# Optimization experiments

Hardware: AMD Instinct MI355X
Metric: run time of the kernel (lower is better)

Reference implementation:

```python
import jax, jax.numpy as jnp
import numpy as np

B, T, D_IN, D_PROJ = 256, 2048, 25, 128


def setup_inputs() -> dict:
    key = jax.random.key(0)
    ks = jax.random.split(key, 7)
    s1 = 1.0 / np.sqrt(D_IN)
    s2 = 1.0 / np.sqrt(D_PROJ)
    return {
        "x": jax.random.normal(ks[0], (B, T, D_IN), dtype=jnp.float32),
        "ln_gamma": jnp.ones((D_IN,), dtype=jnp.float32),
        "ln_beta": jnp.zeros((D_IN,), dtype=jnp.float32),
        "w1": jax.random.uniform(ks[1], (D_IN, D_PROJ), jnp.float32, -s1, s1),
        "b1": jax.random.uniform(ks[2], (D_PROJ,), jnp.float32, -s1, s1),
        "w2": jax.random.uniform(ks[3], (D_PROJ, D_PROJ), jnp.float32, -s2, s2),
        "b2": jax.random.uniform(ks[4], (D_PROJ,), jnp.float32, -s2, s2),
    }


def reference(x, ln_gamma, ln_beta, w1, b1, w2, b2):
    # LayerNorm over last dim (eps=1e-5, torch default)
    mu = jnp.mean(x, axis=-1, keepdims=True)
    var = jnp.mean(jnp.square(x - mu), axis=-1, keepdims=True)
    xn = (x - mu) * jax.lax.rsqrt(var + 1e-5) * ln_gamma + ln_beta
    h = jnp.einsum("btd,dp->btp", xn, w1) + b1
    h = jax.nn.gelu(h, approximate=False)  # torch nn.GELU default = exact erf
    return jnp.einsum("btp,pq->btq", h, w2) + b2
```

## Files before the change

### kernel.cpp

```cpp
#include <hip/hip_runtime.h>
#include <hip/hip_bf16.h>
#include <stdint.h>

#define BT    (256*2048)
#define DIN   25
#define DP    128
#define MTILE 128
#define NBLK  (BT/MTILE)
#define HSTR  136

typedef __attribute__((ext_vector_type(8))) __bf16          bf16x8;
typedef __attribute__((ext_vector_type(8))) unsigned short  u16x8;
typedef __attribute__((ext_vector_type(4))) float           f32x4;

#define SM_H     0
#define SM_XN    34816
#define SM_SMALL (34816 + 8192)
#define SM_BYTES (SM_SMALL + 306*4)

__device__ __forceinline__ unsigned short f2bf(float f) {
  unsigned int u = __float_as_uint(f);
  u += 0x7fffu + ((u >> 16) & 1u);
  return (unsigned short)(u >> 16);
}

__device__ __forceinline__ float gelu_exact(float x) {
  float z  = 0.70710678118654752f * x;
  float az = __builtin_fabsf(z);
  float t  = __builtin_amdgcn_rcpf(1.0f + 0.3275911f * az);
  float p  = t*(0.254829592f + t*(-0.284496736f + t*(1.421413741f +
             t*(-1.453152027f + t*1.061405429f))));
  float e  = __expf(-z*z);
  float erf_az = 1.0f - p*e;
  float erf_z  = (x < 0.f) ? -erf_az : erf_az;
  return 0.5f * x * (1.0f + erf_z);
}

__device__ __forceinline__ void async16(void* lds, const void* g) {
  __builtin_amdgcn_global_load_lds(
      (const __attribute__((address_space(1))) unsigned int*)g,
      (__attribute__((address_space(3)))       unsigned int*)lds, 16, 0, 0);
}

__global__ void prep_kernel(const float* __restrict__ w1, const float* __restrict__ w2,
                            unsigned short* __restrict__ wf) {
  int idx = blockIdx.x * 256 + threadIdx.x;
  if (idx >= 40 * 512) return;
  int f = idx >> 9, r = idx & 511, l = r >> 3, j = r & 7;
  float val;
  if (f < 8) {
    int k = (l >> 4) * 8 + j;
    int n = f * 16 + (l & 15);
    val = (k < DIN) ? w1[k * DP + n] : 0.f;
  } else {
    int g = f - 8, nt = g >> 2, ks = g & 3;
    int k = ks * 32 + (l >> 4) * 8 + j;
    int n = nt * 16 + (l & 15);
    val = w2[k * DP + n];
  }
  wf[idx] = f2bf(val);
}

__global__ __launch_bounds__(256, 2) void fused_kernel(
    const float* __restrict__ x,   const float* __restrict__ gam,
    const float* __restrict__ bet, const float* __restrict__ b1,
    const float* __restrict__ b2,  const unsigned short* __restrict__ wfr,
    float* __restrict__ out) {
  __shared__ __align__(16) unsigned char smem[SM_BYTES];
  const int tid  = threadIdx.x;
  const int lane = tid & 63, w = tid >> 6;
  const int quad = lane >> 4, l15 = lane & 15;
  const long long row0 = (long long)blockIdx.x * MTILE;

  {
    const float* src = x + row0 * DIN;
    for (int c = tid; c < 800; c += 256)
      async16(smem + c * 16, src + c * 4);
  }
  float* sg  = (float*)(smem + SM_SMALL);
  float* sbt = sg + 25;
  float* sb1 = sbt + 25;
  float* sb2 = sb1 + 128;
  if (tid < 128) { sb1[tid] = b1[tid]; sb2[tid] = b2[tid]; }
  if (tid < 25)  { sg[tid] = gam[tid]; sbt[tid] = bet[tid]; }
  __syncthreads();

  if (tid < MTILE) {
    const float* xr = (const float*)smem + tid * DIN;
    float s = 0.f;
#pragma unroll
    for (int j = 0; j < DIN; j++) s += xr[j];
    float mu = s * (1.f / DIN);
    float v = 0.f;
#pragma unroll
    for (int j = 0; j < DIN; j++) { float d = xr[j] - mu; v += d * d; }
    float inv = rsqrtf(v * (1.f / DIN) + 1e-5f);
    int mt = tid >> 4, mr = tid & 15;
    unsigned char* fb = smem + SM_XN + mt * 1024;
#pragma unroll
    for (int q = 0; q < 4; q++) {
      u16x8 pk;
#pragma unroll
      for (int j = 0; j < 8; j++) {
        int k = q * 8 + j;
        float val = (k < DIN) ? ((xr[k] - mu) * inv * sg[k] + sbt[k]) : 0.f;
        pk[j] = f2bf(val);
      }
      *(u16x8*)(fb + (mr + 16 * q) * 16) = pk;
    }
  }
  __syncthreads();

  const unsigned char* wfb = (const unsigned char*)wfr;
  bf16x8 wb1[8];
#pragma unroll
  for (int nt = 0; nt < 8; nt++)
    wb1[nt] = *(const bf16x8*)(wfb + nt * 1024 + lane * 16);

  unsigned short* hb = (unsigned short*)smem;
  const f32x4 zf = {0.f, 0.f, 0.f, 0.f};
#pragma unroll
  for (int mi = 0; mi < 2; mi++) {
    int mt = w * 2 + mi;
    bf16x8 a = *(const bf16x8*)(smem + SM_XN + mt * 1024 + lane * 16);
    f32x4 acc[8];
#pragma unroll
    for (int nt = 0; nt < 8; nt++)
      acc[nt] = __builtin_amdgcn_mfma_f32_16x16x32_bf16(a, wb1[nt], zf, 0, 0, 0);
#pragma unroll
    for (int nt = 0; nt < 8; nt++) {
      float bias = sb1[nt * 16 + l15];
      int col = nt * 16 + l15;
#pragma unroll
      for (int r = 0; r < 4; r++) {
        int row = mt * 16 + quad * 4 + r;
        float hp = acc[nt][r] + bias;
        hb[row * HSTR + col] = f2bf(gelu_exact(hp));
      }
    }
  }
  __syncthreads();

  bf16x8 wb2[2][4];
#pragma unroll
  for (int ni = 0; ni < 2; ni++)
#pragma unroll
    for (int ks = 0; ks < 4; ks++)
      wb2[ni][ks] = *(const bf16x8*)(wfb + 8192 + (((w * 2 + ni) * 4) + ks) * 1024 + lane * 16);

  float bias0 = sb2[(w * 2 + 0) * 16 + l15];
  float bias1 = sb2[(w * 2 + 1) * 16 + l15];

  for (int mt = 0; mt < 8; mt++) {
    f32x4 a0 = zf, a1 = zf;
    f32x4 acc0 = zf, acc1 = zf;
#pragma unroll
    for (int ks = 0; ks < 4; ks++) {
      bf16x8 af = *(const bf16x8*)(smem + (mt * 16 + l15) * (HSTR * 2) + ks * 64 + quad * 16);
      acc0 = __builtin_amdgcn_mfma_f32_16x16x32_bf16(af, wb2[0][ks], acc0, 0, 0, 0);
      acc1 = __builtin_amdgcn_mfma_f32_16x16x32_bf16(af, wb2[1][ks], acc1, 0, 0, 0);
    }
    float* orow = out + (row0 + mt * 16) * DP;
    int c0 = (w * 2 + 0) * 16 + l15;
    int c1 = (w * 2 + 1) * 16 + l15;
#pragma unroll
    for (int r = 0; r < 4; r++) {
      int row = quad * 4 + r;
      orow[row * DP + c0] = acc0[r] + bias0;
      orow[row * DP + c1] = acc1[r] + bias1;
    }
    (void)a0; (void)a1;
  }
}

extern "C" void kernel_launch(void* const* d_in, const int* in_sizes, int n_in,
                              void* d_out, int out_size, void* d_ws, size_t ws_size,
                              hipStream_t stream) {
  const float* x   = (const float*)d_in[0];
  const float* gam = (const float*)d_in[1];
  const float* bet = (const float*)d_in[2];
  const float* w1  = (const float*)d_in[3];
  const float* b1  = (const float*)d_in[4];
  const float* w2  = (const float*)d_in[5];
  const float* b2  = (const float*)d_in[6];
  float* out = (float*)d_out;
  unsigned short* wf = (unsigned short*)d_ws;

  prep_kernel<<<80, 256, 0, stream>>>(w1, w2, wf);
  fused_kernel<<<NBLK, 256, 0, stream>>>(x, gam, bet, b1, b2, wf, out);
}
```

Measured before the change: 328.5 us.

## Make each wave own a 32-token tile and fold LayerNorm affine into weights

Restructures the fused kernel so each of the four waves independently processes 32 tokens in its own LDS slot, removing all block-wide __syncthreads barriers. LayerNorm gamma and beta are folded into W1 and b1 in the prep kernel, so the main kernel only normalizes. Per-wave LDS shrinks, which allows a higher occupancy target (launch_bounds 3). In exchange, W2 fragments are now reloaded from global memory per wave instead of being held by a wave across all row tiles. Output stores now cover all 128 columns per wave rather than two column tiles.

```diff
diff --git a/kernel.cpp b/kernel.cpp
--- a/kernel.cpp
+++ b/kernel.cpp
@@ -1,22 +1,22 @@
 #include <hip/hip_runtime.h>
-#include <hip/hip_bf16.h>
 #include <stdint.h>
 
 #define BT    (256*2048)
 #define DIN   25
 #define DP    128
-#define MTILE 128
-#define NBLK  (BT/MTILE)
-#define HSTR  136
+#define WTOK  32
+#define NBLK  (BT/(4*WTOK))
+#define HS    132
 
 typedef __attribute__((ext_vector_type(8))) __bf16          bf16x8;
 typedef __attribute__((ext_vector_type(8))) unsigned short  u16x8;
 typedef __attribute__((ext_vector_type(4))) float           f32x4;
 
-#define SM_H     0
-#define SM_XN    34816
-#define SM_SMALL (34816 + 8192)
-#define SM_BYTES (SM_SMALL + 306*4)
+#define WSLOT 10496
+#define SMB   (4*WSLOT)
+
+#define WS_W2  8192
+#define WS_B1  40960
 
 __device__ __forceinline__ unsigned short f2bf(float f) {
   unsigned int u = __float_as_uint(f);
@@ -43,133 +43,130 @@
 }
 
 __global__ void prep_kernel(const float* __restrict__ w1, const float* __restrict__ w2,
+                            const float* __restrict__ gam, const float* __restrict__ bet,
+                            const float* __restrict__ b1,
                             unsigned short* __restrict__ wf) {
   int idx = blockIdx.x * 256 + threadIdx.x;
-  if (idx >= 40 * 512) return;
-  int f = idx >> 9, r = idx & 511, l = r >> 3, j = r & 7;
-  float val;
-  if (f < 8) {
-    int k = (l >> 4) * 8 + j;
-    int n = f * 16 + (l & 15);
-    val = (k < DIN) ? w1[k * DP + n] : 0.f;
-  } else {
-    int g = f - 8, nt = g >> 2, ks = g & 3;
-    int k = ks * 32 + (l >> 4) * 8 + j;
-    int n = nt * 16 + (l & 15);
-    val = w2[k * DP + n];
+  if (idx < 40 * 512) {
+    int f = idx >> 9, r = idx & 511, l = r >> 3, j = r & 7;
+    float val;
+    if (f < 8) {
+      int k = (l >> 4) * 8 + j;
+      int n = f * 16 + (l & 15);
+      val = (k < DIN) ? gam[k] * w1[k * DP + n] : 0.f;
+    } else {
+      int g = f - 8, nt = g >> 2, ks = g & 3;
+      int k = ks * 32 + (l >> 4) * 8 + j;
+      int n = nt * 16 + (l & 15);
+      val = w2[k * DP + n];
+    }
+    wf[idx] = f2bf(val);
+  } else if (idx < 40 * 512 + DP) {
+    int n = idx - 40 * 512;
+    float s = b1[n];
+    for (int k = 0; k < DIN; k++) s += bet[k] * w1[k * DP + n];
+    ((float*)((char*)wf + WS_B1))[n] = s;
   }
-  wf[idx] = f2bf(val);
 }
 
-__global__ __launch_bounds__(256, 2) void fused_kernel(
-    const float* __restrict__ x,   const float* __restrict__ gam,
-    const float* __restrict__ bet, const float* __restrict__ b1,
-    const float* __restrict__ b2,  const unsigned short* __restrict__ wfr,
-    float* __restrict__ out) {
-  __shared__ __align__(16) unsigned char smem[SM_BYTES];
+__global__ __launch_bounds__(256, 3) void fused_kernel(
+    const float* __restrict__ x, const float* __restrict__ b2,
+    const unsigned short* __restrict__ wfr, float* __restrict__ out) {
+  __shared__ __align__(16) unsigned char smem[SMB];
   const int tid  = threadIdx.x;
   const int lane = tid & 63, w = tid >> 6;
   const int quad = lane >> 4, l15 = lane & 15;
-  const long long row0 = (long long)blockIdx.x * MTILE;
+  unsigned char* base = smem + w * WSLOT;
+  const long long t0 = ((long long)blockIdx.x * 4 + w) * WTOK;
+  const unsigned char* wfb = (const unsigned char*)wfr;
+  const float* b1p = (const float*)(wfb + WS_B1);
 
   {
-    const float* src = x + row0 * DIN;
-    for (int c = tid; c < 800; c += 256)
-      async16(smem + c * 16, src + c * 4);
+    const float* src = x + t0 * DIN;
+    for (int c = lane; c < 200; c += 64)
+      async16(base + c * 16, src + c * 4);
   }
-  float* sg  = (float*)(smem + SM_SMALL);
-  float* sbt = sg + 25;
-  float* sb1 = sbt + 25;
-  float* sb2 = sb1 + 128;
-  if (tid < 128) { sb1[tid] = b1[tid]; sb2[tid] = b2[tid]; }
-  if (tid < 25)  { sg[tid] = gam[tid]; sbt[tid] = bet[tid]; }
-  __syncthreads();
-
-  if (tid < MTILE) {
-    const float* xr = (const float*)smem + tid * DIN;
-    float s = 0.f;
+  float b1v[8], b2v[8];
 #pragma unroll
-    for (int j = 0; j < DIN; j++) s += xr[j];
-    float mu = s * (1.f / DIN);
-    float v = 0.f;
-#pragma unroll
-    for (int j = 0; j < DIN; j++) { float d = xr[j] - mu; v += d * d; }
-    float inv = rsqrtf(v * (1.f / DIN) + 1e-5f);
-    int mt = tid >> 4, mr = tid & 15;
-    unsigned char* fb = smem + SM_XN + mt * 1024;
-#pragma unroll
-    for (int q = 0; q < 4; q++) {
-      u16x8 pk;
-#pragma unroll
-      for (int j = 0; j < 8; j++) {
-        int k = q * 8 + j;
-        float val = (k < DIN) ? ((xr[k] - mu) * inv * sg[k] + sbt[k]) : 0.f;
-        pk[j] = f2bf(val);
-      }
-      *(u16x8*)(fb + (mr + 16 * q) * 16) = pk;
-    }
-  }
-  __syncthreads();
-
-  const unsigned char* wfb = (const unsigned char*)wfr;
+  for (int nt = 0; nt < 8; nt++) { b1v[nt] = b1p[nt*16 + l15]; b2v[nt] = b2[nt*16 + l15]; }
   bf16x8 wb1[8];
 #pragma unroll
   for (int nt = 0; nt < 8; nt++)
     wb1[nt] = *(const bf16x8*)(wfb + nt * 1024 + lane * 16);
 
-  unsigned short* hb = (unsigned short*)smem;
-  const f32x4 zf = {0.f, 0.f, 0.f, 0.f};
+  asm volatile("s_waitcnt vmcnt(0)" ::: "memory");
+
+  {
+    const int tt = lane & 31, half = lane >> 5;
+    const float* xr = (const float*)(base + tt * (DIN * 4));
+    float xv[DIN];
+    float s = 0.f;
 #pragma unroll
-  for (int mi = 0; mi < 2; mi++) {
-    int mt = w * 2 + mi;
-    bf16x8 a = *(const bf16x8*)(smem + SM_XN + mt * 1024 + lane * 16);
-    f32x4 acc[8];
+    for (int j = 0; j < DIN; j++) { xv[j] = xr[j]; s += xv[j]; }
+    float mu = s * (1.f / DIN);
+    float v = 0.f;
 #pragma unroll
-    for (int nt = 0; nt < 8; nt++)
-      acc[nt] = __builtin_amdgcn_mfma_f32_16x16x32_bf16(a, wb1[nt], zf, 0, 0, 0);
+    for (int j = 0; j < DIN; j++) { float d = xv[j] - mu; v += d * d; }
+    float inv = rsqrtf(v * (1.f / DIN) + 1e-5f);
+    const int mt = tt >> 4, mr = tt & 15;
+    unsigned char* fb = base + 8448 + mt * 1024;
 #pragma unroll
-    for (int nt = 0; nt < 8; nt++) {
-      float bias = sb1[nt * 16 + l15];
-      int col = nt * 16 + l15;
+    for (int qq = 0; qq < 2; qq++) {
+      int q = 2 * half + qq;
+      u16x8 pk;
 #pragma unroll
-      for (int r = 0; r < 4; r++) {
-        int row = mt * 16 + quad * 4 + r;
-        float hp = acc[nt][r] + bias;
-        hb[row * HSTR + col] = f2bf(gelu_exact(hp));
+      for (int j = 0; j < 8; j++) {
+        int k = q * 8 + j;
+        pk[j] = (k < DIN) ? f2bf((xv[k] - mu) * inv) : (unsigned short)0;
       }
+      *(u16x8*)(fb + (mr + 16 * q) * 16) = pk;
     }
   }
-  __syncthreads();
 
-  bf16x8 wb2[2][4];
+  const f32x4 zf = {0.f, 0.f, 0.f, 0.f};
+  bf16x8 a0 = *(const bf16x8*)(base + 8448 + lane * 16);
+  bf16x8 a1 = *(const bf16x8*)(base + 8448 + 1024 + lane * 16);
+  unsigned short* hb = (unsigned short*)base;
 #pragma unroll
-  for (int ni = 0; ni < 2; ni++)
-#pragma unroll
-    for (int ks = 0; ks < 4; ks++)
-      wb2[ni][ks] = *(const bf16x8*)(wfb + 8192 + (((w * 2 + ni) * 4) + ks) * 1024 + lane * 16);
-
-  float bias0 = sb2[(w * 2 + 0) * 16 + l15];
-  float bias1 = sb2[(w * 2 + 1) * 16 + l15];
-
-  for (int mt = 0; mt < 8; mt++) {
-    f32x4 a0 = zf, a1 = zf;
-    f32x4 acc0 = zf, acc1 = zf;
-#pragma unroll
-    for (int ks = 0; ks < 4; ks++) {
-      bf16x8 af = *(const bf16x8*)(smem + (mt * 16 + l15) * (HSTR * 2) + ks * 64 + quad * 16);
-      acc0 = __builtin_amdgcn_mfma_f32_16x16x32_bf16(af, wb2[0][ks], acc0, 0, 0, 0);
-      acc1 = __builtin_amdgcn_mfma_f32_16x16x32_bf16(af, wb2[1][ks], acc1, 0, 0, 0);
-    }
-    float* orow = out + (row0 + mt * 16) * DP;
-    int c0 = (w * 2 + 0) * 16 + l15;
-    int c1 = (w * 2 + 1) * 16 + l15;
+  for (int nt = 0; nt < 8; nt++) {
+    f32x4 c0 = __builtin_amdgcn_mfma_f32_16x16x32_bf16(a0, wb1[nt], zf, 0, 0, 0);
+    f32x4 c1 = __builtin_amdgcn_mfma_f32_16x16x32_bf16(a1, wb1[nt], zf, 0, 0, 0);
+    int col = nt * 16 + l15;
 #pragma unroll
     for (int r = 0; r < 4; r++) {
       int row = quad * 4 + r;
-      orow[row * DP + c0] = acc0[r] + bias0;
-      orow[row * DP + c1] = acc1[r] + bias1;
+      hb[row * HS + col]        = f2bf(gelu_exact(c0[r] + b1v[nt]));
+      hb[(16 + row) * HS + col] = f2bf(gelu_exact(c1[r] + b1v[nt]));
     }
-    (void)a0; (void)a1;
+  }
+
+  bf16x8 aA[2][4];
+#pragma unroll
+  for (int mi = 0; mi < 2; mi++)
+#pragma unroll
+    for (int ks = 0; ks < 4; ks++)
+      aA[mi][ks] = *(const bf16x8*)(base + (mi*16 + l15) * (HS*2) + ks*64 + quad*16);
+
+#pragma unroll 2
+  for (int nt = 0; nt < 8; nt++) {
+    bf16x8 wf2[4];
+#pragma unroll
+    for (int ks = 0; ks < 4; ks++)
+      wf2[ks] = *(const bf16x8*)(wfb + WS_W2 + ((nt*4 + ks) * 1024) + lane * 16);
+    f32x4 c0 = zf, c1 = zf;
+#pragma unroll
+    for (int ks = 0; ks < 4; ks++) {
+      c0 = __builtin_amdgcn_mfma_f32_16x16x32_bf16(aA[0][ks], wf2[ks], c0, 0, 0, 0);
+      c1 = __builtin_amdgcn_mfma_f32_16x16x32_bf16(aA[1][ks], wf2[ks], c1, 0, 0, 0);
+    }
+    int col = nt * 16 + l15;
+    float bias = b2v[nt];
+#pragma unroll
+    for (int r = 0; r < 4; r++) {
+      int row = quad * 4 + r;
+      out[(t0 + row) * DP + col]      = c0[r] + bias;
+      out[(t0 + 16 + row) * DP + col] = c1[r] + bias;
+    }
   }
 }
 
@@ -186,6 +183,6 @@
   float* out = (float*)d_out;
   unsigned short* wf = (unsigned short*)d_ws;
 
-  prep_kernel<<<80, 256, 0, stream>>>(w1, w2, wf);
-  fused_kernel<<<NBLK, 256, 0, stream>>>(x, gam, bet, b1, b2, wf, out);
+  prep_kernel<<<81, 256, 0, stream>>>(w1, w2, gam, bet, b1, wf);
+  fused_kernel<<<NBLK, 256, 0, stream>>>(x, b2, wf, out);
 }
```

Measured after the change: 341.0 us. 1.04x slower.
